# Performance work log

Hardware: AMD Instinct MI355X
Metric: run time of the kernel (lower is better)

Reference implementation:

```python
import jax, jax.numpy as jnp
import numpy as np

B, L, D_MODEL, H, D_K, D_V, C = 4, 2048, 512, 8, 64, 64, 5
LN_EPS = 1e-5


def setup_inputs() -> dict:
    key = jax.random.key(0)
    ks = jax.random.split(key, 9)
    u_k = min(int(C * np.log(L)), L)  # 38
    s = 1.0 / np.sqrt(D_MODEL)
    return {
        "input_Q": jax.random.normal(ks[0], (B, L, D_MODEL), jnp.float32),
        "input_K": jax.random.normal(ks[1], (B, L, D_MODEL), jnp.float32),
        "input_V": jax.random.normal(ks[2], (B, L, D_MODEL), jnp.float32),
        "W_Q": jax.random.normal(ks[3], (D_MODEL, H * D_K), jnp.float32) * s,
        "W_K": jax.random.normal(ks[4], (D_MODEL, H * D_K), jnp.float32) * s,
        "W_V": jax.random.normal(ks[5], (D_MODEL, H * D_V), jnp.float32) * s,
        "W_fc": jax.random.normal(ks[6], (H * D_V, D_MODEL), jnp.float32) * (1.0 / np.sqrt(H * D_V)),
        "ln_gamma": jnp.ones((D_MODEL,), jnp.float32),
        "ln_beta": jnp.zeros((D_MODEL,), jnp.float32),
        "index_sample": jax.random.randint(ks[7], (L, u_k), 0, L, jnp.int32),
    }


def reference(input_Q, input_K, input_V, W_Q, W_K, W_V, W_fc, ln_gamma, ln_beta, index_sample):
    Bb, L_Q, _ = input_Q.shape
    L_K = input_K.shape[1]
    u_q = min(int(C * np.log(L_Q)), L_Q)  # n_top queries kept

    # projections -> (B, H, L, d)
    Q = (input_Q @ W_Q).reshape(Bb, L_Q, H, D_K).transpose(0, 2, 1, 3)
    K = (input_K @ W_K).reshape(Bb, L_K, H, D_K).transpose(0, 2, 1, 3)
    V = (input_V @ W_V).reshape(Bb, L_K, H, D_V).transpose(0, 2, 1, 3)

    # sampled QK scores: gather u_k random keys per query position
    K_sample = K[:, :, index_sample, :]                      # (B,H,L_Q,u_k,d_k)
    QK_sample = jnp.einsum('bhqe,bhqke->bhqk', Q, K_sample)  # (B,H,L_Q,u_k)

    # sparsity measure M = max - mean, top-u_q queries
    M = QK_sample.max(axis=-1) - QK_sample.mean(axis=-1)     # (B,H,L_Q)
    _, idx = jax.lax.top_k(M, u_q)                           # (B,H,u_q)

    # attention only for selected queries
    Q_sel = jnp.take_along_axis(Q, idx[..., None], axis=2)   # (B,H,u_q,d_k)
    scores = jnp.einsum('bhue,bhke->bhuk', Q_sel, K) / np.sqrt(D_K)
    attn = jax.nn.softmax(scores, axis=-1)
    values = jnp.einsum('bhuk,bhkd->bhud', attn, V)          # (B,H,u_q,d_v)

    # initial context = mean of V (attn_mask is None), scatter selected rows
    context = jnp.broadcast_to(V.mean(axis=2, keepdims=True), (Bb, H, L_Q, D_V))
    bb = jnp.arange(Bb)[:, None, None]
    hh = jnp.arange(H)[None, :, None]
    context = context.at[bb, hh, idx].set(values)

    context = context.transpose(0, 2, 1, 3).reshape(Bb, L_Q, H * D_V)
    out = context @ W_fc                                     # dropout p=0.0

    y = out + input_Q
    mu = y.mean(axis=-1, keepdims=True)
    var = jnp.mean(jnp.square(y - mu), axis=-1, keepdims=True)
    y = (y - mu) / jnp.sqrt(var + LN_EPS) * ln_gamma + ln_beta
    return y, idx
```

## Files before the change

### kernel.cpp

```cpp
#include <hip/hip_runtime.h>
#include <hip/hip_bf16.h>

#define NB 4
#define NL 2048
#define NH 8
#define NDM 512
#define ND 64
#define KSPLIT 4
#define QB 8

typedef __attribute__((ext_vector_type(8))) short short8b;
typedef __attribute__((ext_vector_type(4))) float f32x4;

__global__ void samp_flag_init(int* __restrict__ flag) {
  if (threadIdx.x == 0 && blockIdx.x == 0) *flag = 0;
}
__global__ void samp_probe(const int* __restrict__ sampAsInt, int* __restrict__ flag, int nwords) {
  const int g = blockIdx.x * 256 + threadIdx.x;
  if (g < nwords) {
    unsigned v = (unsigned)sampAsInt[g];
    if (v >= 2048u) atomicOr(flag, 1);
  }
}
__global__ void samp_convert(const void* __restrict__ samp, const int* __restrict__ flag,
                             int* __restrict__ sampI, int n) {
  const int g = blockIdx.x * 256 + threadIdx.x;
  if (g >= n) return;
  int v;
  if (*flag == 0) v = ((const int*)samp)[g];
  else            v = (int)(((const float*)samp)[g]);
  if (v < 0) v = 0;
  if (v > NL - 1) v = NL - 1;
  sampI[g] = v;
}

__global__ void wconv(const float* __restrict__ W, unsigned short* __restrict__ WT) {
  const int g = blockIdx.x * 256 + threadIdx.x;
  const int k = g >> 9, c = g & 511;
  __hip_bfloat16 hb = __float2bfloat16(W[(size_t)k * 512 + c]);
  WT[(size_t)c * 512 + k] = *reinterpret_cast<unsigned short*>(&hb);
}

__global__ __launch_bounds__(256, 4) void proj3(
    const float* __restrict__ AQ, const float* __restrict__ AK,
    const float* __restrict__ wQm, const float* __restrict__ wKm,
    int gh0, float* __restrict__ Qc, float* __restrict__ Kc) {
  __shared__ float As_[32 * 132];
  __shared__ float Ws_[32 * 68];
  const int tid = threadIdx.x;
  const int bm = blockIdx.x;
  const int hl = blockIdx.y;
  const int mat = blockIdx.z;
  const int bh = gh0 + hl;
  const int b = bh >> 3, h = bh & 7;
  const float* A = (mat == 0) ? AQ : AK;
  const float* W = (mat == 0) ? wQm : wKm;
  float* D = (mat == 0) ? Qc : Kc;
  const float* Ab = A + (size_t)b * NL * NDM;
  const int colbase = h * 64;
  const int tm = tid >> 4, tn = tid & 15;
  float acc[8][4] = {};
  for (int k0 = 0; k0 < 512; k0 += 32) {
#pragma unroll
    for (int i = 0; i < 4; ++i) {
      int s = tid + i * 256;
      int r = s >> 3, c4 = (s & 7) * 4;
      float4 v = *reinterpret_cast<const float4*>(Ab + (size_t)(bm * 128 + r) * 512 + k0 + c4);
      As_[(c4 + 0) * 132 + r] = v.x;
      As_[(c4 + 1) * 132 + r] = v.y;
      As_[(c4 + 2) * 132 + r] = v.z;
      As_[(c4 + 3) * 132 + r] = v.w;
    }
#pragma unroll
    for (int i = 0; i < 2; ++i) {
      int s = tid + i * 256;
      int r = s >> 4, c4 = (s & 15) * 4;
      *reinterpret_cast<float4*>(&Ws_[r * 68 + c4]) =
          *reinterpret_cast<const float4*>(W + (size_t)(k0 + r) * 512 + colbase + c4);
    }
    __syncthreads();
#pragma unroll
    for (int kk = 0; kk < 32; ++kk) {
      float4 a0 = *reinterpret_cast<const float4*>(&As_[kk * 132 + tm * 4]);
      float4 a1 = *reinterpret_cast<const float4*>(&As_[kk * 132 + 64 + tm * 4]);
      float4 w  = *reinterpret_cast<const float4*>(&Ws_[kk * 68 + tn * 4]);
      float a[8] = {a0.x, a0.y, a0.z, a0.w, a1.x, a1.y, a1.z, a1.w};
      float wv[4] = {w.x, w.y, w.z, w.w};
#pragma unroll
      for (int ii = 0; ii < 8; ++ii)
#pragma unroll
        for (int jj = 0; jj < 4; ++jj) acc[ii][jj] += a[ii] * wv[jj];
    }
    __syncthreads();
  }
#pragma unroll
  for (int ii = 0; ii < 8; ++ii) {
    int row = bm * 128 + ((ii < 4) ? (tm * 4 + ii) : (64 + tm * 4 + (ii - 4)));
    float4 v = make_float4(acc[ii][0], acc[ii][1], acc[ii][2], acc[ii][3]);
    *reinterpret_cast<float4*>(D + ((size_t)hl * NL + row) * ND + tn * 4) = v;
  }
}

__global__ __launch_bounds__(256) void projV_mfma(
    const float* __restrict__ AV, const unsigned short* __restrict__ WT,
    int gh0, float* __restrict__ Vc) {
  const int wv = threadIdx.x >> 6, l = threadIdx.x & 63;
  const int bm = blockIdx.x;
  const int hl = blockIdx.y;
  const int bh = gh0 + hl;
  const int b = bh >> 3, h = bh & 7;
  const float* Ab = AV + (size_t)b * NL * NDM;
  const int row = bm * 64 + wv * 16 + (l & 15);
  const int kg = (l >> 4) * 8;
  f32x4 acc0 = {}, acc1 = {}, acc2 = {}, acc3 = {};
  for (int k0 = 0; k0 < 512; k0 += 32) {
    const float* ap = Ab + (size_t)row * 512 + k0 + kg;
    short8b af;
#pragma unroll
    for (int j = 0; j < 8; ++j) {
      __hip_bfloat16 hb = __float2bfloat16(ap[j]);
      af[j] = *reinterpret_cast<short*>(&hb);
    }
    const unsigned short* wp = WT + (size_t)(h * 64 + (l & 15)) * 512 + k0 + kg;
    short8b b0 = *reinterpret_cast<const short8b*>(wp);
    short8b b1 = *reinterpret_cast<const short8b*>(wp + 16 * 512);
    short8b b2 = *reinterpret_cast<const short8b*>(wp + 32 * 512);
    short8b b3 = *reinterpret_cast<const short8b*>(wp + 48 * 512);
    acc0 = __builtin_amdgcn_mfma_f32_16x16x32_bf16(af, b0, acc0, 0, 0, 0);
    acc1 = __builtin_amdgcn_mfma_f32_16x16x32_bf16(af, b1, acc1, 0, 0, 0);
    acc2 = __builtin_amdgcn_mfma_f32_16x16x32_bf16(af, b2, acc2, 0, 0, 0);
    acc3 = __builtin_amdgcn_mfma_f32_16x16x32_bf16(af, b3, acc3, 0, 0, 0);
  }
  const int rbase = bm * 64 + wv * 16 + (l >> 4) * 4;
  const int col = l & 15;
#pragma unroll
  for (int j = 0; j < 4; ++j) {
    size_t o = ((size_t)hl * NL + rbase + j) * ND + col;
    Vc[o] = acc0[j];
    Vc[o + 16] = acc1[j];
    Vc[o + 32] = acc2[j];
    Vc[o + 48] = acc3[j];
  }
}

template <int UK>
__global__ __launch_bounds__(256) void sample_scores_t(
    const float* __restrict__ Q, const float* __restrict__ K,
    const int* __restrict__ sampI, float* __restrict__ M) {
  __shared__ float KsAll[4][UK * 66];
  __shared__ float QsAll[4][68];
  const int wv = threadIdx.x >> 6, l = threadIdx.x & 63;
  const int gq = blockIdx.x * 4 + wv;
  const int hl = gq >> 11;
  const int q = gq & 2047;
  float* Ks = KsAll[wv];
  float* Qs = QsAll[wv];
  const float* Kb = K + (size_t)hl * NL * ND;
  Qs[l] = Q[(size_t)gq * ND + l];
  const int base = __builtin_amdgcn_readfirstlane(q) * UK;
#pragma unroll
  for (int r = 0; r < UK; ++r) {
    int kk = sampI[base + r] & (NL - 1);
    Ks[r * 66 + l] = Kb[(size_t)kk * ND + l];
  }
  __syncthreads();
  const int myk = (l < UK) ? l : (UK - 1);
  float acc = 0.f;
#pragma unroll
  for (int j = 0; j < 32; ++j) {
    float2 kv = *reinterpret_cast<const float2*>(&Ks[myk * 66 + 2 * j]);
    float2 qv = *reinterpret_cast<const float2*>(&Qs[2 * j]);
    acc += kv.x * qv.x + kv.y * qv.y;
  }
  float mval = (l < UK) ? acc : -1e30f;
  float sval = (l < UK) ? acc : 0.f;
#pragma unroll
  for (int o = 32; o; o >>= 1) {
    mval = fmaxf(mval, __shfl_xor(mval, o, 64));
    sval += __shfl_xor(sval, o, 64);
  }
  if (l == 0) M[gq] = mval - sval * (1.f / (float)UK);
}

__global__ void sample_scores_gen(const float* __restrict__ Q, const float* __restrict__ K,
                                  const int* __restrict__ sampI, float* __restrict__ M, int uk) {
  const int wave = threadIdx.x >> 6, lane = threadIdx.x & 63;
  const int gq = blockIdx.x * 4 + wave;
  const int hl = gq >> 11;
  const int q = gq & 2047;
  const float qv = Q[(size_t)gq * ND + lane];
  const float* Kbase = K + (size_t)hl * NL * ND;
  float mx = -1e30f, sm = 0.f;
  for (int k = 0; k < uk; ++k) {
    int kidx = sampI[q * uk + k] & (NL - 1);
    float p = qv * Kbase[(size_t)kidx * ND + lane];
#pragma unroll
    for (int o = 32; o; o >>= 1) p += __shfl_xor(p, o, 64);
    mx = fmaxf(mx, p);
    sm += p;
  }
  if (lane == 0) M[gq] = mx - sm / (float)uk;
}

__global__ void topk_kernel(const float* __restrict__ M, int* __restrict__ idxo,
                            float* __restrict__ outIdx, int uq) {
  __shared__ float mv[2048];
  __shared__ float bwv[4];
  __shared__ int bwi[4];
  const int bh = blockIdx.x, t = threadIdx.x;
  for (int i = 0; i < 8; ++i) mv[t + i * 256] = M[(size_t)bh * 2048 + t + i * 256];
  __syncthreads();
  for (int it = 0; it < uq; ++it) {
    float best = -1e38f; int bidx = 1 << 30;
#pragma unroll
    for (int i = 0; i < 8; ++i) {
      int id = t + i * 256;
      float v = mv[id];
      if (v > best || (v == best && id < bidx)) { best = v; bidx = id; }
    }
#pragma unroll
    for (int o = 32; o; o >>= 1) {
      float ov = __shfl_xor(best, o, 64);
      int oi = __shfl_xor(bidx, o, 64);
      if (ov > best || (ov == best && oi < bidx)) { best = ov; bidx = oi; }
    }
    if ((t & 63) == 0) { bwv[t >> 6] = best; bwi[t >> 6] = bidx; }
    __syncthreads();
    if (t == 0) {
      float bb = bwv[0]; int bi2 = bwi[0];
#pragma unroll
      for (int w = 1; w < 4; ++w) {
        if (bwv[w] > bb || (bwv[w] == bb && bwi[w] < bi2)) { bb = bwv[w]; bi2 = bwi[w]; }
      }
      int sel = bi2 & (NL - 1);
      idxo[bh * uq + it] = sel;
      outIdx[bh * uq + it] = (float)sel;
      mv[sel] = -1e38f;
    }
    __syncthreads();
  }
}

__global__ void vmean_part(const float* __restrict__ V, float* __restrict__ Vmp) {
  __shared__ float red[256];
  const int hl = blockIdx.x, seg = blockIdx.y;
  const int t = threadIdx.x, d = t & 63, sl = t >> 6;
  const float* Vb = V + (size_t)hl * NL * ND;
  float s = 0.f;
  for (int k = seg * 256 + sl; k < seg * 256 + 256; k += 4) s += Vb[(size_t)k * ND + d];
  red[t] = s;
  __syncthreads();
  if (sl == 0)
    Vmp[((size_t)hl * 8 + seg) * ND + d] = red[d] + red[64 + d] + red[128 + d] + red[192 + d];
}
__global__ void vmean_final(const float* __restrict__ Vmp, float* __restrict__ Vmg) {
  const int hl = blockIdx.x, d = threadIdx.x;
  float s = 0.f;
#pragma unroll
  for (int seg = 0; seg < 8; ++seg) s += Vmp[((size_t)hl * 8 + seg) * ND + d];
  Vmg[hl * ND + d] = s * (1.f / 2048.f);
}

__global__ __launch_bounds__(256) void attn_part(
    const float* __restrict__ Qw, const float* __restrict__ Kw, const float* __restrict__ Vw,
    const int* __restrict__ idxo, float* __restrict__ pacc, float* __restrict__ pml, int uq) {
  __shared__ float Qs[QB][68];
  __shared__ float Ks[64][68];
  __shared__ float Vs[64][68];
  __shared__ float sc[QB][66];
  __shared__ float accs[QB][68];
  const int hl = blockIdx.x, qg = blockIdx.y, ks = blockIdx.z;
  const int t = threadIdx.x;
#pragma unroll
  for (int i = 0; i < 2; ++i) {
    int s = t + i * 256;
    int q = s >> 6, d = s & 63;
    int u = qg * QB + q;
    float v = 0.f;
    if (u < uq) {
      int qi = idxo[hl * uq + u] & (NL - 1);
      v = Qw[((size_t)hl * NL + qi) * ND + d];
    }
    Qs[q][d] = v;
    accs[q][d] = 0.f;
  }
  float m_run = -1e30f, l_run = 0.f;
  const int q2 = t >> 5, ln = t & 31;
  __syncthreads();
  const int kbeg = ks * (NL / KSPLIT);
  for (int k0 = kbeg; k0 < kbeg + NL / KSPLIT; k0 += 64) {
#pragma unroll
    for (int i = 0; i < 4; ++i) {
      int s = t + i * 256;
      int r = s >> 4, c4 = (s & 15) * 4;
      *reinterpret_cast<float4*>(&Ks[r][c4]) =
          *reinterpret_cast<const float4*>(Kw + ((size_t)hl * NL + k0 + r) * ND + c4);
      *reinterpret_cast<float4*>(&Vs[r][c4]) =
          *reinterpret_cast<const float4*>(Vw + ((size_t)hl * NL + k0 + r) * ND + c4);
    }
    __syncthreads();
    {
      const int q = t & 7, kk = t >> 3;
      float d0 = 0.f, d1 = 0.f;
#pragma unroll
      for (int dd = 0; dd < 64; dd += 4) {
        float4 qv = *reinterpret_cast<const float4*>(&Qs[q][dd]);
        float4 ka = *reinterpret_cast<const float4*>(&Ks[kk][dd]);
        float4 kb = *reinterpret_cast<const float4*>(&Ks[kk + 32][dd]);
        d0 += qv.x * ka.x + qv.y * ka.y + qv.z * ka.z + qv.w * ka.w;
        d1 += qv.x * kb.x + qv.y * kb.y + qv.z * kb.z + qv.w * kb.w;
      }
      sc[q][kk] = d0 * 0.125f;
      sc[q][kk + 32] = d1 * 0.125f;
    }
    __syncthreads();
    {
      float s0 = sc[q2][ln], s1 = sc[q2][ln + 32];
      float tmax = fmaxf(s0, s1);
#pragma unroll
      for (int o = 16; o; o >>= 1) tmax = fmaxf(tmax, __shfl_xor(tmax, o, 64));
      float mnew = fmaxf(m_run, tmax);
      float scl = __expf(m_run - mnew);
      float p0 = __expf(s0 - mnew), p1 = __expf(s1 - mnew);
      float tsum = p0 + p1;
#pragma unroll
      for (int o = 16; o; o >>= 1) tsum += __shfl_xor(tsum, o, 64);
      l_run = l_run * scl + tsum;
      m_run = mnew;
      sc[q2][ln] = p0; sc[q2][ln + 32] = p1;
      float a0 = accs[q2][2 * ln] * scl, a1 = accs[q2][2 * ln + 1] * scl;
#pragma unroll 8
      for (int k = 0; k < 64; ++k) {
        float p = sc[q2][k];
        a0 += p * Vs[k][2 * ln];
        a1 += p * Vs[k][2 * ln + 1];
      }
      accs[q2][2 * ln] = a0; accs[q2][2 * ln + 1] = a1;
    }
    __syncthreads();
  }
  const int u = qg * QB + q2;
  if (u < uq) {
    size_t g = ((size_t)hl * uq + u) * KSPLIT + ks;
    pacc[g * ND + 2 * ln] = accs[q2][2 * ln];
    pacc[g * ND + 2 * ln + 1] = accs[q2][2 * ln + 1];
    if (ln == 0) { pml[g * 2] = m_run; pml[g * 2 + 1] = l_run; }
  }
}

__global__ void attn_merge(const float* __restrict__ pacc, const float* __restrict__ pml,
                           float* __restrict__ vals, int uq) {
  const int g = blockIdx.x;
  const int d = threadIdx.x;
  float mstar = -1e30f;
#pragma unroll
  for (int s = 0; s < KSPLIT; ++s) mstar = fmaxf(mstar, pml[((size_t)g * KSPLIT + s) * 2]);
  float num = 0.f, den = 0.f;
#pragma unroll
  for (int s = 0; s < KSPLIT; ++s) {
    float e = __expf(pml[((size_t)g * KSPLIT + s) * 2] - mstar);
    den += e * pml[((size_t)g * KSPLIT + s) * 2 + 1];
    num += e * pacc[((size_t)g * KSPLIT + s) * ND + d];
  }
  vals[(size_t)g * ND + d] = num / den;
}

__global__ void selmap_init(short* __restrict__ selmap) {
  const int g = blockIdx.x * 256 + threadIdx.x;
  selmap[g] = -1;
  selmap[g + 32768] = -1;
}
__global__ void selmap_fill(const int* __restrict__ idxo, short* __restrict__ selmap, int uq) {
  const int g = blockIdx.x * 256 + threadIdx.x;
  if (g >= NB * NH * uq) return;
  const int bh = g / uq, u = g - bh * uq;
  const int b = bh >> 3, h = bh & 7;
  const int l = idxo[g] & (NL - 1);
  selmap[((size_t)b * NL + l) * NH + h] = (short)u;
}

__global__ void base_gemm(const float* __restrict__ Vm, const float* __restrict__ Wfc,
                          float* __restrict__ base) {
  __shared__ float vm[512];
  const int b = blockIdx.x, t = threadIdx.x;
  vm[t] = Vm[b * 512 + t];
  vm[t + 256] = Vm[b * 512 + t + 256];
  __syncthreads();
  const int c0 = blockIdx.y * 256 + t;
  float acc = 0.f;
  for (int k = 0; k < 512; ++k) acc += vm[k] * Wfc[(size_t)k * 512 + c0];
  base[b * 512 + c0] = acc;
}

__global__ void corr_gemm(const float* __restrict__ vals, const float* __restrict__ Vm,
                          const float* __restrict__ Wfc, float* __restrict__ corr, int uq) {
  __shared__ float diff[64];
  const int g = blockIdx.x, t = threadIdx.x;
  const int bh = g / uq;
  const int h = bh & 7;
  if (t < 64) diff[t] = vals[(size_t)g * 64 + t] - Vm[bh * 64 + t];
  __syncthreads();
  float a0 = 0.f, a1 = 0.f;
#pragma unroll
  for (int d = 0; d < 64; ++d) {
    a0 += diff[d] * Wfc[(size_t)(h * 64 + d) * 512 + t];
    a1 += diff[d] * Wfc[(size_t)(h * 64 + d) * 512 + t + 256];
  }
  corr[(size_t)g * 512 + t] = a0;
  corr[(size_t)g * 512 + t + 256] = a1;
}

__global__ void ln_fused(const float* __restrict__ base, const float* __restrict__ resid,
                         const float* __restrict__ corr, const short* __restrict__ selmap,
                         const float* __restrict__ gamma, const float* __restrict__ beta,
                         float* __restrict__ out, int uq) {
  __shared__ float red[256];
  const int row = blockIdx.x, t = threadIdx.x;
  const int b = row >> 11;
  float y0 = base[b * 512 + t] + resid[(size_t)row * 512 + t];
  float y1 = base[b * 512 + 256 + t] + resid[(size_t)row * 512 + 256 + t];
#pragma unroll
  for (int h = 0; h < NH; ++h) {
    int s = selmap[(size_t)row * NH + h];
    if (s >= 0 && s < uq) {
      const float* cp = corr + (size_t)((b * NH + h) * uq + s) * 512;
      y0 += cp[t];
      y1 += cp[t + 256];
    }
  }
  red[t] = y0 + y1;
  __syncthreads();
  for (int s = 128; s; s >>= 1) { if (t < s) red[t] += red[t + s]; __syncthreads(); }
  const float mu = red[0] * (1.f / 512.f);
  __syncthreads();
  const float d0 = y0 - mu, d1 = y1 - mu;
  red[t] = d0 * d0 + d1 * d1;
  __syncthreads();
  for (int s = 128; s; s >>= 1) { if (t < s) red[t] += red[t + s]; __syncthreads(); }
  const float rs = rsqrtf(red[0] * (1.f / 512.f) + 1e-5f);
  __syncthreads();
  out[(size_t)row * 512 + t] = d0 * rs * gamma[t] + beta[t];
  out[(size_t)row * 512 + 256 + t] = d1 * rs * gamma[256 + t] + beta[256 + t];
}

extern "C" void kernel_launch(void* const* d_in, const int* in_sizes, int n_in,
                              void* d_out, int out_size, void* d_ws, size_t ws_size,
                              hipStream_t stream) {
  const float* inQ = (const float*)d_in[0];
  const float* inK = (const float*)d_in[1];
  const float* inV = (const float*)d_in[2];
  const float* wQ = (const float*)d_in[3];
  const float* wK = (const float*)d_in[4];
  const float* wV = (const float*)d_in[5];
  const float* wFC = (const float*)d_in[6];
  const float* gamma = (const float*)d_in[7];
  const float* beta = (const float*)d_in[8];
  const void* samp = d_in[9];

  const int nsamp = in_sizes[9];
  const int uk = nsamp / NL;
  const int uq = uk;
  const int nqg = (uq + QB - 1) / QB;

  if (out_size < NB * NL * NDM + NB * NH * uq) return;

  const size_t perH = 3 * 131072 + 2048 + (size_t)uq * KSPLIT * 64 + (size_t)uq * KSPLIT * 2 + 8 * 64;
  const size_t fixed = (size_t)32 * uq * 64 + 2048 + 2048 + (size_t)32 * uq * 512
                     + (size_t)32 * uq + 32768 + (size_t)nsamp + 131072 + 256;
  int hcg = 0;
  for (int c = 32; c >= 1; c >>= 1) {
    if ((perH * (size_t)c + fixed + 256) * 4ull <= ws_size) { hcg = c; break; }
  }
  if (hcg == 0) return;

  float* ws = (float*)d_ws;
  float* Qc = ws;
  float* Kc = Qc + (size_t)hcg * 131072;
  float* Vc = Kc + (size_t)hcg * 131072;
  float* Mb = Vc + (size_t)hcg * 131072;
  float* pacc = Mb + (size_t)hcg * 2048;
  float* pml = pacc + (size_t)hcg * uq * KSPLIT * 64;
  float* Vmp = pml + (size_t)hcg * uq * KSPLIT * 2;
  float* vals = Vmp + (size_t)hcg * 8 * 64;
  float* Vm = vals + (size_t)32 * uq * 64;
  float* base = Vm + 2048;
  float* corr = base + 2048;
  int* idxo = (int*)(corr + (size_t)32 * uq * 512);
  short* selmap = (short*)(idxo + (size_t)32 * uq);
  int* sampI = (int*)(selmap + 65536);
  int* flag = sampI + nsamp;
  unsigned short* WTv = (unsigned short*)(flag + 64);

  float* out = (float*)d_out;
  float* outIdx = out + (size_t)NB * NL * NDM;

  const int nwords = nsamp / 2;
  samp_flag_init<<<1, 64, 0, stream>>>(flag);
  samp_probe<<<(nwords + 255) / 256, 256, 0, stream>>>((const int*)samp, flag, nwords);
  samp_convert<<<(nsamp + 255) / 256, 256, 0, stream>>>(samp, flag, sampI, nsamp);
  wconv<<<1024, 256, 0, stream>>>(wV, WTv);

  for (int gh0 = 0; gh0 < NB * NH; gh0 += hcg) {
    proj3<<<dim3(16, hcg, 2), 256, 0, stream>>>(inQ, inK, wQ, wK, gh0, Qc, Kc);
    projV_mfma<<<dim3(32, hcg), 256, 0, stream>>>(inV, WTv, gh0, Vc);
    if (uk == 38)
      sample_scores_t<38><<<hcg * NL / 4, 256, 0, stream>>>(Qc, Kc, sampI, Mb);
    else
      sample_scores_gen<<<hcg * NL / 4, 256, 0, stream>>>(Qc, Kc, sampI, Mb, uk);
    topk_kernel<<<hcg, 256, 0, stream>>>(Mb, idxo + (size_t)gh0 * uq,
                                         outIdx + (size_t)gh0 * uq, uq);
    vmean_part<<<dim3(hcg, 8), 256, 0, stream>>>(Vc, Vmp);
    vmean_final<<<hcg, 64, 0, stream>>>(Vmp, Vm + (size_t)gh0 * ND);
    attn_part<<<dim3(hcg, nqg, KSPLIT), 256, 0, stream>>>(Qc, Kc, Vc,
                                                          idxo + (size_t)gh0 * uq,
                                                          pacc, pml, uq);
    attn_merge<<<hcg * uq, 64, 0, stream>>>(pacc, pml, vals + (size_t)gh0 * uq * ND, uq);
  }

  selmap_init<<<NB * NL * NH / 2 / 256, 256, 0, stream>>>(selmap);
  selmap_fill<<<(NB * NH * uq + 255) / 256, 256, 0, stream>>>(idxo, selmap, uq);
  base_gemm<<<dim3(NB, 2), 256, 0, stream>>>(Vm, wFC, base);
  corr_gemm<<<NB * NH * uq, 256, 0, stream>>>(vals, Vm, wFC, corr, uq);
  ln_fused<<<NB * NL, 256, 0, stream>>>(base, inQ, corr, selmap, gamma, beta, out, uq);
}
```

Measured before the change: 370.9 us.

## Compute V mean from input column means; prefetch and swizzle proj3 tiles

The mean of V is now computed algebraically as mean(input_V) @ W_V, using a column-mean kernel and a small GEMV launched once before the head loop. This replaces the per-head reduction over projected V. Separately, proj3 now prefetches the next k-tile of A and W into registers while the current tile is computed, and XOR-swizzles its shared-memory A layout to reduce bank conflicts on the transposed stores. The cost is extra workspace for the partial column sums and higher register pressure in proj3, and the V mean is summed in a different order than before.

```diff
diff --git a/kernel.cpp b/kernel.cpp
--- a/kernel.cpp
+++ b/kernel.cpp
@@ -39,6 +39,35 @@
   const int k = g >> 9, c = g & 511;
   __hip_bfloat16 hb = __float2bfloat16(W[(size_t)k * 512 + c]);
   WT[(size_t)c * 512 + k] = *reinterpret_cast<unsigned short*>(&hb);
+}
+
+__global__ void vmean_colmean(const float* __restrict__ inV, float* __restrict__ parts) {
+  const int b = blockIdx.x, seg = blockIdx.y, t = threadIdx.x;
+  const float* p = inV + ((size_t)b * NL + seg * 32) * NDM;
+  float s0 = 0.f, s1 = 0.f;
+  for (int r = 0; r < 32; ++r) {
+    s0 += p[(size_t)r * NDM + t];
+    s1 += p[(size_t)r * NDM + 256 + t];
+  }
+  parts[((size_t)b * 64 + seg) * NDM + t] = s0;
+  parts[((size_t)b * 64 + seg) * NDM + 256 + t] = s1;
+}
+__global__ void vmean_gemm(const float* __restrict__ parts, const float* __restrict__ Wv,
+                           float* __restrict__ Vm) {
+  __shared__ float cm[512];
+  const int b = blockIdx.x, t = threadIdx.x;
+  float a0 = 0.f, a1 = 0.f;
+  for (int g = 0; g < 64; ++g) {
+    a0 += parts[((size_t)b * 64 + g) * NDM + t];
+    a1 += parts[((size_t)b * 64 + g) * NDM + 256 + t];
+  }
+  cm[t] = a0 * (1.f / 2048.f);
+  cm[t + 256] = a1 * (1.f / 2048.f);
+  __syncthreads();
+  const int c0 = blockIdx.y * 256 + t;
+  float acc = 0.f;
+  for (int k = 0; k < 512; ++k) acc += cm[k] * Wv[(size_t)k * NDM + c0];
+  Vm[b * 512 + c0] = acc;
 }
 
 __global__ __launch_bounds__(256, 4) void proj3(
@@ -60,29 +89,58 @@
   const int colbase = h * 64;
   const int tm = tid >> 4, tn = tid & 15;
   float acc[8][4] = {};
+  f32x4 ra[4], rw[2];
+#pragma unroll
+  for (int i = 0; i < 4; ++i) {
+    int s = tid + i * 256;
+    int r = s >> 3, c4 = (s & 7) * 4;
+    ra[i] = *reinterpret_cast<const f32x4*>(Ab + (size_t)(bm * 128 + r) * 512 + c4);
+  }
+#pragma unroll
+  for (int i = 0; i < 2; ++i) {
+    int s = tid + i * 256;
+    int r = s >> 4, c4 = (s & 15) * 4;
+    rw[i] = *reinterpret_cast<const f32x4*>(W + (size_t)r * 512 + colbase + c4);
+  }
   for (int k0 = 0; k0 < 512; k0 += 32) {
 #pragma unroll
     for (int i = 0; i < 4; ++i) {
       int s = tid + i * 256;
       int r = s >> 3, c4 = (s & 7) * 4;
-      float4 v = *reinterpret_cast<const float4*>(Ab + (size_t)(bm * 128 + r) * 512 + k0 + c4);
-      As_[(c4 + 0) * 132 + r] = v.x;
-      As_[(c4 + 1) * 132 + r] = v.y;
-      As_[(c4 + 2) * 132 + r] = v.z;
-      As_[(c4 + 3) * 132 + r] = v.w;
+#pragma unroll
+      for (int j = 0; j < 4; ++j) {
+        int c = c4 + j;
+        int rs = r ^ (((c >> 2) & 3) << 3);
+        As_[c * 132 + rs] = ra[i][j];
+      }
     }
 #pragma unroll
     for (int i = 0; i < 2; ++i) {
       int s = tid + i * 256;
       int r = s >> 4, c4 = (s & 15) * 4;
-      *reinterpret_cast<float4*>(&Ws_[r * 68 + c4]) =
-          *reinterpret_cast<const float4*>(W + (size_t)(k0 + r) * 512 + colbase + c4);
-    }
-    __syncthreads();
+      *reinterpret_cast<f32x4*>(&Ws_[r * 68 + c4]) = rw[i];
+    }
+    __syncthreads();
+    if (k0 + 32 < 512) {
+#pragma unroll
+      for (int i = 0; i < 4; ++i) {
+        int s = tid + i * 256;
+        int r = s >> 3, c4 = (s & 7) * 4;
+        ra[i] = *reinterpret_cast<const f32x4*>(Ab + (size_t)(bm * 128 + r) * 512 + k0 + 32 + c4);
+      }
+#pragma unroll
+      for (int i = 0; i < 2; ++i) {
+        int s = tid + i * 256;
+        int r = s >> 4, c4 = (s & 15) * 4;
+        rw[i] = *reinterpret_cast<const f32x4*>(W + (size_t)(k0 + 32 + r) * 512 + colbase + c4);
+      }
+    }
 #pragma unroll
     for (int kk = 0; kk < 32; ++kk) {
-      float4 a0 = *reinterpret_cast<const float4*>(&As_[kk * 132 + tm * 4]);
-      float4 a1 = *reinterpret_cast<const float4*>(&As_[kk * 132 + 64 + tm * 4]);
+      const int sw = ((kk >> 2) & 3) << 3;
+      const int mbase = (tm * 4) ^ sw;
+      float4 a0 = *reinterpret_cast<const float4*>(&As_[kk * 132 + mbase]);
+      float4 a1 = *reinterpret_cast<const float4*>(&As_[kk * 132 + 64 + mbase]);
       float4 w  = *reinterpret_cast<const float4*>(&Ws_[kk * 68 + tn * 4]);
       float a[8] = {a0.x, a0.y, a0.z, a0.w, a1.x, a1.y, a1.z, a1.w};
       float wv[4] = {w.x, w.y, w.z, w.w};
@@ -241,26 +299,6 @@
   }
 }
 
-__global__ void vmean_part(const float* __restrict__ V, float* __restrict__ Vmp) {
-  __shared__ float red[256];
-  const int hl = blockIdx.x, seg = blockIdx.y;
-  const int t = threadIdx.x, d = t & 63, sl = t >> 6;
-  const float* Vb = V + (size_t)hl * NL * ND;
-  float s = 0.f;
-  for (int k = seg * 256 + sl; k < seg * 256 + 256; k += 4) s += Vb[(size_t)k * ND + d];
-  red[t] = s;
-  __syncthreads();
-  if (sl == 0)
-    Vmp[((size_t)hl * 8 + seg) * ND + d] = red[d] + red[64 + d] + red[128 + d] + red[192 + d];
-}
-__global__ void vmean_final(const float* __restrict__ Vmp, float* __restrict__ Vmg) {
-  const int hl = blockIdx.x, d = threadIdx.x;
-  float s = 0.f;
-#pragma unroll
-  for (int seg = 0; seg < 8; ++seg) s += Vmp[((size_t)hl * 8 + seg) * ND + d];
-  Vmg[hl * ND + d] = s * (1.f / 2048.f);
-}
-
 __global__ __launch_bounds__(256) void attn_part(
     const float* __restrict__ Qw, const float* __restrict__ Kw, const float* __restrict__ Vw,
     const int* __restrict__ idxo, float* __restrict__ pacc, float* __restrict__ pml, int uq) {
@@ -464,9 +502,9 @@
 
   if (out_size < NB * NL * NDM + NB * NH * uq) return;
 
-  const size_t perH = 3 * 131072 + 2048 + (size_t)uq * KSPLIT * 64 + (size_t)uq * KSPLIT * 2 + 8 * 64;
+  const size_t perH = 3 * 131072 + 2048 + (size_t)uq * KSPLIT * 64 + (size_t)uq * KSPLIT * 2;
   const size_t fixed = (size_t)32 * uq * 64 + 2048 + 2048 + (size_t)32 * uq * 512
-                     + (size_t)32 * uq + 32768 + (size_t)nsamp + 131072 + 256;
+                     + (size_t)32 * uq + 32768 + (size_t)nsamp + 131072 + 131072 + 256;
   int hcg = 0;
   for (int c = 32; c >= 1; c >>= 1) {
     if ((perH * (size_t)c + fixed + 256) * 4ull <= ws_size) { hcg = c; break; }
@@ -480,8 +518,7 @@
   float* Mb = Vc + (size_t)hcg * 131072;
   float* pacc = Mb + (size_t)hcg * 2048;
   float* pml = pacc + (size_t)hcg * uq * KSPLIT * 64;
-  float* Vmp = pml + (size_t)hcg * uq * KSPLIT * 2;
-  float* vals = Vmp + (size_t)hcg * 8 * 64;
+  float* vals = pml + (size_t)hcg * uq * KSPLIT * 2;
   float* Vm = vals + (size_t)32 * uq * 64;
   float* base = Vm + 2048;
   float* corr = base + 2048;
@@ -490,6 +527,7 @@
   int* sampI = (int*)(selmap + 65536);
   int* flag = sampI + nsamp;
   unsigned short* WTv = (unsigned short*)(flag + 64);
+  float* vparts = (float*)(WTv + 262144);
 
   float* out = (float*)d_out;
   float* outIdx = out + (size_t)NB * NL * NDM;
@@ -499,6 +537,8 @@
   samp_probe<<<(nwords + 255) / 256, 256, 0, stream>>>((const int*)samp, flag, nwords);
   samp_convert<<<(nsamp + 255) / 256, 256, 0, stream>>>(samp, flag, sampI, nsamp);
   wconv<<<1024, 256, 0, stream>>>(wV, WTv);
+  vmean_colmean<<<dim3(NB, 64), 256, 0, stream>>>(inV, vparts);
+  vmean_gemm<<<dim3(NB, 2), 256, 0, stream>>>(vparts, wV, Vm);
 
   for (int gh0 = 0; gh0 < NB * NH; gh0 += hcg) {
     proj3<<<dim3(16, hcg, 2), 256, 0, stream>>>(inQ, inK, wQ, wK, gh0, Qc, Kc);
@@ -509,8 +549,6 @@
       sample_scores_gen<<<hcg * NL / 4, 256, 0, stream>>>(Qc, Kc, sampI, Mb, uk);
     topk_kernel<<<hcg, 256, 0, stream>>>(Mb, idxo + (size_t)gh0 * uq,
                                          outIdx + (size_t)gh0 * uq, uq);
-    vmean_part<<<dim3(hcg, 8), 256, 0, stream>>>(Vc, Vmp);
-    vmean_final<<<hcg, 64, 0, stream>>>(Vmp, Vm + (size_t)gh0 * ND);
     attn_part<<<dim3(hcg, nqg, KSPLIT), 256, 0, stream>>>(Qc, Kc, Vc,
                                                           idxo + (size_t)gh0 * uq,
                                                           pacc, pml, uq);
```

Result: slower. 444.7 us (+19.9%).
